# Kernel tuning notes

Hardware: AMD Instinct MI355X
Metric: run time of the kernel (lower is better)

The kernel has to match this reference:

```python
import jax, jax.numpy as jnp
import numpy as np

V, D, K = 400000, 300, 10

def setup_inputs() -> dict:
    key = jax.random.key(0)
    k1, k2 = jax.random.split(key)
    word2vec = jax.random.normal(k1, (V, D), dtype=jnp.float32)  # embedding table
    w = jax.random.normal(k2, (D,), dtype=jnp.float32)           # query vector
    return {"word2vec": word2vec, "w": w, "k": K}

def reference(word2vec, w, k):
    # cosine similarity: (word2vec @ w) / (||rows|| * ||w||), matching torch eps placement
    dots = word2vec @ w                                          # [V]
    row_norms = jnp.sqrt(jnp.sum(word2vec * word2vec, axis=1) + 1e-9)  # [V]
    q_norm = jnp.sqrt(jnp.sum(w * w))
    cos = dots / (row_norms * q_norm)                            # [V]
    vals, topk = jax.lax.top_k(cos, k)                           # top-k neighbors
    return vals, topk
```

## Files before the change

kernel.cpp:

```cpp
#include <hip/hip_runtime.h>

#define D    300
#define NF4  75
#define K    10
#define WPB  4
#define GPB  16
#define NBLOCKS 2048
#define NGROUPS (NBLOCKS * GPB)

#define P2_BLOCKS  256
#define P2_THREADS 1024
#define P2_CPT     2
#define NCAND      (P2_BLOCKS * K)
#define F_CPT      3

typedef float f32x4 __attribute__((ext_vector_type(4)));

__device__ __forceinline__ f32x4 ntload(const f32x4* p) {
    return __builtin_nontemporal_load(p);
}

__device__ __forceinline__ float d4(f32x4 a, f32x4 b) {
    return a[0]*b[0] + a[1]*b[1] + a[2]*b[2] + a[3]*b[3];
}

#define RED16(x) { x += __shfl_xor(x, 8, 64); x += __shfl_xor(x, 4, 64); \
                   x += __shfl_xor(x, 2, 64); x += __shfl_xor(x, 1, 64); }

__global__ __launch_bounds__(256) void cos_all(
    const float* __restrict__ emb, const float* __restrict__ wvec,
    float* __restrict__ score, int V, int s)
{
    const int tid  = threadIdx.x;
    const int lane = tid & 63;
    const int wid  = tid >> 6;
    const int l16  = lane & 15;
    const int rg   = lane >> 4;
    const bool tl  = (l16 < NF4 - 64);

    const f32x4* w4p = (const f32x4*)wvec;
    f32x4 w0 = w4p[l16];
    f32x4 w1 = w4p[l16 + 16];
    f32x4 w2 = w4p[l16 + 32];
    f32x4 w3 = w4p[l16 + 48];
    f32x4 w4t = 0.f;
    if (tl) w4t = w4p[l16 + 64];

    float qsq = d4(w0,w0)+d4(w1,w1)+d4(w2,w2)+d4(w3,w3)+d4(w4t,w4t);
    RED16(qsq);
    const float qn = sqrtf(qsq);

    const int g0 = (blockIdx.x * WPB + wid) * 4 + rg;
    const size_t stepF4 = (size_t)s * NF4;

    const f32x4* p = (const f32x4*)emb + (size_t)g0 * NF4 + l16;

    for (int r = g0; r < V; r += s, p += stepF4) {
        f32x4 a0 = ntload(p);
        f32x4 a1 = ntload(p + 16);
        f32x4 a2 = ntload(p + 32);
        f32x4 a3 = ntload(p + 48);
        f32x4 a4 = 0.f;
        if (tl) a4 = ntload(p + 64);

        float da = d4(a0,w0) + d4(a1,w1);
        float db = d4(a2,w2) + d4(a3,w3) + d4(a4,w4t);
        float sa = d4(a0,a0) + d4(a1,a1);
        float sb = d4(a2,a2) + d4(a3,a3) + d4(a4,a4);
        float dot = da + db;
        float sq  = sa + sb;

        RED16(dot); RED16(sq);
        float c = dot / (sqrtf(sq + 1e-9f) * qn);
        if (l16 == 0) score[r] = c;
    }
}

__global__ __launch_bounds__(P2_THREADS) void block_topk(
    const float* __restrict__ score, int V,
    float* __restrict__ cand_v, int* __restrict__ cand_i)
{
    __shared__ float rv[16];
    __shared__ int   rp[16];
    __shared__ int   s_bp;

    const int tid  = threadIdx.x;
    const int lane = tid & 63;
    const int wid  = tid >> 6;
    const int per  = (V + P2_BLOCKS - 1) / P2_BLOCKS;
    const int base = blockIdx.x * per;

    float v[P2_CPT];
    #pragma unroll
    for (int t = 0; t < P2_CPT; ++t) {
        int i = tid + t * P2_THREADS;
        v[t] = (i < per && base + i < V) ? score[base + i] : -3e38f;
    }

    for (int p = 0; p < K; ++p) {
        float bestv = -3e38f; int bestpos = 0x7fffffff;
        #pragma unroll
        for (int t = 0; t < P2_CPT; ++t) {
            if (v[t] > bestv) { bestv = v[t]; bestpos = tid + t * P2_THREADS; }
        }
        #pragma unroll
        for (int m = 32; m >= 1; m >>= 1) {
            float ov = __shfl_xor(bestv, m, 64);
            int   op = __shfl_xor(bestpos, m, 64);
            if (ov > bestv || (ov == bestv && op < bestpos)) { bestv = ov; bestpos = op; }
        }
        if (lane == 0) { rv[wid] = bestv; rp[wid] = bestpos; }
        __syncthreads();
        if (tid == 0) {
            float bv = rv[0]; int bp = rp[0];
            for (int i = 1; i < 16; ++i)
                if (rv[i] > bv || (rv[i] == bv && rp[i] < bp)) { bv = rv[i]; bp = rp[i]; }
            cand_v[blockIdx.x*K + p] = bv;
            cand_i[blockIdx.x*K + p] = base + bp;
            s_bp = bp;
        }
        __syncthreads();
        const int wbp = s_bp;
        #pragma unroll
        for (int t = 0; t < P2_CPT; ++t) {
            if (tid + t * P2_THREADS == wbp) v[t] = -3e38f;
        }
        __syncthreads();
    }
}

__global__ __launch_bounds__(P2_THREADS) void final_topk(
    const float* __restrict__ cand_v, const int* __restrict__ cand_i,
    float* __restrict__ out)
{
    __shared__ float rv[16];
    __shared__ int   rp[16];
    __shared__ int   s_bp;

    const int tid  = threadIdx.x;
    const int lane = tid & 63;
    const int wid  = tid >> 6;

    float v[F_CPT];
    #pragma unroll
    for (int t = 0; t < F_CPT; ++t) {
        int i = tid + t * P2_THREADS;
        v[t] = (i < NCAND) ? cand_v[i] : -3e38f;
    }

    for (int p = 0; p < K; ++p) {
        float bestv = -3e38f; int bestpos = 0x7fffffff;
        #pragma unroll
        for (int t = 0; t < F_CPT; ++t) {
            if (v[t] > bestv) { bestv = v[t]; bestpos = tid + t * P2_THREADS; }
        }
        #pragma unroll
        for (int m = 32; m >= 1; m >>= 1) {
            float ov = __shfl_xor(bestv, m, 64);
            int   op = __shfl_xor(bestpos, m, 64);
            if (ov > bestv || (ov == bestv && op < bestpos)) { bestv = ov; bestpos = op; }
        }
        if (lane == 0) { rv[wid] = bestv; rp[wid] = bestpos; }
        __syncthreads();
        if (tid == 0) {
            float bv = rv[0]; int bp = rp[0];
            for (int i = 1; i < 16; ++i)
                if (rv[i] > bv || (rv[i] == bv && rp[i] < bp)) { bv = rv[i]; bp = rp[i]; }
            out[p]     = bv;
            out[K + p] = (float)cand_i[bp];
            s_bp = bp;
        }
        __syncthreads();
        const int wbp = s_bp;
        #pragma unroll
        for (int t = 0; t < F_CPT; ++t) {
            if (tid + t * P2_THREADS == wbp) v[t] = -3e38f;
        }
        __syncthreads();
    }
}

extern "C" void kernel_launch(void* const* d_in, const int* in_sizes, int n_in,
                              void* d_out, int out_size, void* d_ws, size_t ws_size,
                              hipStream_t stream) {
    const float* emb  = (const float*)d_in[0];
    const float* wvec = (const float*)d_in[1];
    const int V = in_sizes[0] / D;

    float* score  = (float*)d_ws;
    float* cand_v = score + V;
    int*   cand_i = (int*)(cand_v + NCAND);

    cos_all<<<NBLOCKS, 256, 0, stream>>>(emb, wvec, score, V, NGROUPS);
    block_topk<<<P2_BLOCKS, P2_THREADS, 0, stream>>>(score, V, cand_v, cand_i);
    final_topk<<<1, P2_THREADS, 0, stream>>>(cand_v, cand_i, (float*)d_out);
}
```

Baseline: 122.4 us.

## Stream embedding rows through double-buffered LDS via direct global-to-LDS loads

Replaces the grid-stride register-load scan with a persistent 256-block kernel. Each block copies 64-row chunks into double-buffered shared memory using global_load_lds, then computes dot products and norms from LDS while the next chunk is in flight. The aim is to overlap HBM streaming with compute and to issue fully coalesced 1KB loads. In exchange the grid drops from 2048 to 256 blocks, each using 150KB of LDS, so occupancy falls to one block per CU. The nontemporal hint is also lost, and a full vmcnt(0) wait plus a barrier runs on every chunk.

```diff
diff --git a/kernel.cpp b/kernel.cpp
--- a/kernel.cpp
+++ b/kernel.cpp
@@ -1,12 +1,14 @@
 #include <hip/hip_runtime.h>
+#include <stdint.h>
 
 #define D    300
-#define NF4  75
 #define K    10
-#define WPB  4
-#define GPB  16
-#define NBLOCKS 2048
-#define NGROUPS (NBLOCKS * GPB)
+
+#define CHUNK_ROWS   64
+#define CHUNK_FLOATS (CHUNK_ROWS * D)
+#define CHUNK_BYTES  (CHUNK_FLOATS * 4)
+#define NLOADS       75
+#define NBLK         256
 
 #define P2_BLOCKS  256
 #define P2_THREADS 1024
@@ -16,10 +18,6 @@
 
 typedef float f32x4 __attribute__((ext_vector_type(4)));
 
-__device__ __forceinline__ f32x4 ntload(const f32x4* p) {
-    return __builtin_nontemporal_load(p);
-}
-
 __device__ __forceinline__ float d4(f32x4 a, f32x4 b) {
     return a[0]*b[0] + a[1]*b[1] + a[2]*b[2] + a[3]*b[3];
 }
@@ -27,16 +25,17 @@
 #define RED16(x) { x += __shfl_xor(x, 8, 64); x += __shfl_xor(x, 4, 64); \
                    x += __shfl_xor(x, 2, 64); x += __shfl_xor(x, 1, 64); }
 
-__global__ __launch_bounds__(256) void cos_all(
+__global__ __launch_bounds__(256) void cos_all_lds(
     const float* __restrict__ emb, const float* __restrict__ wvec,
-    float* __restrict__ score, int V, int s)
+    float* __restrict__ score, int V)
 {
+    extern __shared__ float lds[];
     const int tid  = threadIdx.x;
     const int lane = tid & 63;
     const int wid  = tid >> 6;
     const int l16  = lane & 15;
-    const int rg   = lane >> 4;
-    const bool tl  = (l16 < NF4 - 64);
+    const int grp  = tid >> 4;
+    const bool tl  = (l16 < 11);
 
     const f32x4* w4p = (const f32x4*)wvec;
     f32x4 w0 = w4p[l16];
@@ -50,29 +49,74 @@
     RED16(qsq);
     const float qn = sqrtf(qsq);
 
-    const int g0 = (blockIdx.x * WPB + wid) * 4 + rg;
-    const size_t stepF4 = (size_t)s * NF4;
-
-    const f32x4* p = (const f32x4*)emb + (size_t)g0 * NF4 + l16;
-
-    for (int r = g0; r < V; r += s, p += stepF4) {
-        f32x4 a0 = ntload(p);
-        f32x4 a1 = ntload(p + 16);
-        f32x4 a2 = ntload(p + 32);
-        f32x4 a3 = ntload(p + 48);
+    const int nchunks = V / CHUNK_ROWS;
+
+#define STAGE(c, b)                                                            \
+    {                                                                          \
+        const uint8_t* gbase = (const uint8_t*)emb + (size_t)(c) * CHUNK_BYTES;\
+        uint8_t* lbase = (uint8_t*)lds + (size_t)(b) * CHUNK_BYTES;            \
+        for (int j = wid; j < NLOADS; j += 4) {                                \
+            __builtin_amdgcn_global_load_lds(                                  \
+                (const __attribute__((address_space(1))) void*)                \
+                    (gbase + j * 1024 + lane * 16),                            \
+                (__attribute__((address_space(3))) void*)(lbase + j * 1024),   \
+                16, 0, 0);                                                     \
+        }                                                                      \
+    }
+
+    int c   = blockIdx.x;
+    int cur = 0;
+    if (c < nchunks) STAGE(c, 0);
+
+    for (; c < nchunks; c += NBLK, cur ^= 1) {
+        asm volatile("s_waitcnt vmcnt(0)" ::: "memory");
+        __syncthreads();
+        const int cn = c + NBLK;
+        if (cn < nchunks) STAGE(cn, cur ^ 1);
+
+        const float* lb = lds + cur * CHUNK_FLOATS;
+        #pragma unroll
+        for (int rr = 0; rr < 4; ++rr) {
+            const int row = grp * 4 + rr;
+            const f32x4* rp = (const f32x4*)(lb + row * D);
+            f32x4 a0 = rp[l16];
+            f32x4 a1 = rp[l16 + 16];
+            f32x4 a2 = rp[l16 + 32];
+            f32x4 a3 = rp[l16 + 48];
+            f32x4 a4 = 0.f;
+            if (tl) a4 = rp[l16 + 64];
+
+            float da = d4(a0,w0) + d4(a1,w1);
+            float db = d4(a2,w2) + d4(a3,w3) + d4(a4,w4t);
+            float sa = d4(a0,a0) + d4(a1,a1);
+            float sb = d4(a2,a2) + d4(a3,a3) + d4(a4,a4);
+            float dot = da + db;
+            float sq  = sa + sb;
+            RED16(dot); RED16(sq);
+            float cv = dot / (sqrtf(sq + 1e-9f) * qn);
+            if (l16 == 0) score[c * CHUNK_ROWS + row] = cv;
+        }
+    }
+#undef STAGE
+
+    const int rem0 = nchunks * CHUNK_ROWS;
+    for (int r = rem0 + blockIdx.x * 16 + grp; r < V; r += NBLK * 16) {
+        const f32x4* rp = (const f32x4*)(emb + (size_t)r * D);
+        f32x4 a0 = rp[l16];
+        f32x4 a1 = rp[l16 + 16];
+        f32x4 a2 = rp[l16 + 32];
+        f32x4 a3 = rp[l16 + 48];
         f32x4 a4 = 0.f;
-        if (tl) a4 = ntload(p + 64);
-
+        if (tl) a4 = rp[l16 + 64];
         float da = d4(a0,w0) + d4(a1,w1);
         float db = d4(a2,w2) + d4(a3,w3) + d4(a4,w4t);
         float sa = d4(a0,a0) + d4(a1,a1);
         float sb = d4(a2,a2) + d4(a3,a3) + d4(a4,a4);
         float dot = da + db;
         float sq  = sa + sb;
-
         RED16(dot); RED16(sq);
-        float c = dot / (sqrtf(sq + 1e-9f) * qn);
-        if (l16 == 0) score[r] = c;
+        float cv = dot / (sqrtf(sq + 1e-9f) * qn);
+        if (l16 == 0) score[r] = cv;
     }
 }
 
@@ -191,7 +235,7 @@
     float* cand_v = score + V;
     int*   cand_i = (int*)(cand_v + NCAND);
 
-    cos_all<<<NBLOCKS, 256, 0, stream>>>(emb, wvec, score, V, NGROUPS);
+    cos_all_lds<<<NBLK, 256, 2 * CHUNK_BYTES, stream>>>(emb, wvec, score, V);
     block_topk<<<P2_BLOCKS, P2_THREADS, 0, stream>>>(score, V, cand_v, cand_i);
     final_topk<<<1, P2_THREADS, 0, stream>>>(cand_v, cand_i, (float*)d_out);
 }
```

Result: slower. 133.0 us (+8.7%).
